# Kernel tuning notes

Measured on AMD Instinct MI355X. Metric: run time of the kernel, lower is better.

## Reference

```python
import jax, jax.numpy as jnp
import numpy as np

N_CLASS = 126
C = N_CLASS + 2      # START tag = C-2, STOP tag = C-1
B, T = 128, 512
NEG_BIG = -100000.0  # transition mask value from the torch init
NEG_INIT = -10000.0  # alpha init value


def setup_inputs() -> dict:
    key = jax.random.key(0)
    k1, k2, k3, k4 = jax.random.split(key, 4)
    feats = jax.random.normal(k1, (B, T, C), dtype=jnp.float32)
    # contiguous prefix masks (valid lengths in [1, T]) as the CRF scoring assumes
    lengths = jax.random.randint(k2, (B,), 1, T + 1)
    mask = (jnp.arange(T)[None, :] < lengths[:, None]).astype(jnp.int32)
    tags = jax.random.randint(k3, (B, T), 0, N_CLASS)  # real tags exclude START/STOP
    trans = jax.random.normal(k4, (C, C), dtype=jnp.float32)
    trans = trans.at[:, C - 2].set(NEG_BIG)  # nothing transitions INTO start
    trans = trans.at[C - 1, :].set(NEG_BIG)  # nothing transitions OUT of stop
    return {"feats": feats, "mask": mask, "tags": tags, "transitions": trans}


def _forward_alg_batch(feats, mask, trans):
    # log-partition via (logsumexp, +) semiring scan over time
    Bc, Tc, Cc = feats.shape
    alpha0 = jnp.full((Bc, Cc), NEG_INIT, feats.dtype).at[:, Cc - 2].set(0.0)
    maskb = mask.astype(bool)

    def step(alpha, xs):
        feat_t, m_t = xs                                   # [B,C], [B]
        smat = alpha[:, :, None] + feat_t[:, None, :] + trans[None]  # [B,C,C]: i->j
        new = jax.nn.logsumexp(smat, axis=1)               # [B,C]
        return jnp.where(m_t[:, None], new, alpha), None

    alpha, _ = jax.lax.scan(
        step, alpha0, (jnp.swapaxes(feats, 0, 1), jnp.swapaxes(maskb, 0, 1))
    )
    last = jax.nn.logsumexp(alpha + trans[:, Cc - 1][None, :], axis=1)  # to STOP
    return jnp.sum(last)


def _score_sentence_batch(feats, tags, mask, trans):
    Bc, Tc, Cc = feats.shape
    seq_len = mask.astype(jnp.int32).sum(1)                # [B]
    r = jnp.arange(Bc)
    start = jnp.full((Bc, 1), Cc - 2, tags.dtype)
    stop = jnp.full((Bc, 1), Cc - 1, tags.dtype)
    pad_start = jnp.concatenate([start, tags], axis=1)     # [B,T+1]
    pad_stop = jnp.concatenate([tags, stop], axis=1)       # [B,T+1]
    pad_stop = pad_stop.at[r, seq_len].set(Cc - 1)         # transition to STOP at end
    t = trans[pad_start, pad_stop]                          # [B,T+1]
    t_score = jnp.sum(jnp.cumsum(t, axis=1)[r, seq_len])
    f = jnp.take_along_axis(feats, tags[:, :, None], axis=2)[..., 0]  # [B,T]
    f_score = jnp.sum(jnp.where(mask.astype(bool), f, 0.0))
    return t_score + f_score


def reference(feats, mask, tags, transitions):
    # CRFTagger.calculate_loss with use_crf=True: NLL / batch_size
    nll = _forward_alg_batch(feats, mask, transitions) - _score_sentence_batch(
        feats, tags, mask, transitions
    )
    return nll / feats.shape[0]
```

## Files before the change

### kernel.cpp

```cpp
#include <hip/hip_runtime.h>


#define BB   128
#define TT   512
#define CC   128
#define NTHR 512
#define PF   4
#define WS_STRIDE 320

typedef float v2f __attribute__((ext_vector_type(2)));

__device__ __forceinline__ void bar_nodrain() {
    asm volatile("s_waitcnt lgkmcnt(0)\n\ts_barrier" ::: "memory");
}

template<int CTRL>
__device__ __forceinline__ float dpp_xadd(float x) {
    const int y = __builtin_amdgcn_update_dpp(0, __float_as_int(x), CTRL, 0xF, 0xF, true);
    return x + __int_as_float(y);
}

__device__ __forceinline__ float red8(float x) {
    x = dpp_xadd<0xB1>(x);
    x = dpp_xadd<0x4E>(x);
    x = dpp_xadd<0x141>(x);
    return x;
}

__global__ __launch_bounds__(NTHR) void crf_scan(
    const float* __restrict__ feats,
    const int*   __restrict__ mask,
    const int*   __restrict__ tags,
    const float* __restrict__ trans,
    float*       __restrict__ ws)
{
    const int bb  = blockIdx.x >> 1;
    const int dir = blockIdx.x & 1;
    const int tid = threadIdx.x;
    const int jp  = tid >> 3;
    const int sub = tid & 7;
    const int j0  = jp * 2;
    const int j1  = j0 + 1;
    const int wid = tid >> 6;

    __shared__ __align__(16) float buf[2][CC];
    __shared__ float wred[8];

    const int myM = mask[bb * TT + tid];
    const int len = __syncthreads_count(myM);

    if (dir == 0) {
        float sc = 0.0f;
        if (myM) {
            const int tg = tags[bb * TT + tid];
            sc += feats[((size_t)(bb * TT + tid)) * CC + tg];
            sc += (tid == 0) ? trans[(CC - 2) * CC + tg]
                             : trans[tags[bb * TT + tid - 1] * CC + tg];
            const int nm = (tid == TT - 1) ? 0 : mask[bb * TT + tid + 1];
            if (!nm) sc += trans[tg * CC + (CC - 1)];
        }
        #pragma unroll
        for (int o = 1; o <= 32; o <<= 1) sc += __shfl_xor(sc, o);
        if ((tid & 63) == 0) wred[wid] = sc;
        __syncthreads();
        if (tid == 0) {
            float s = 0.0f;
            #pragma unroll
            for (int k = 0; k < 8; ++k) s += wred[k];
            atomicAdd(&ws[1], s);
        }
    }

    const int M      = len >> 1;
    const int nB     = len - M;
    const int nSteps = dir ? nB : M;

    const float* fb = feats + (size_t)bb * TT * CC;

    const int s2 = sub >> 1;
    int kkA[4];
    v2f F0v[8], F1v[8];
    #pragma unroll
    for (int k = 0; k < 4; ++k) {
        const int kk = (k + s2) & 3;
        kkA[k] = kk;
        const int r = sub * 16 + kk * 4;
        if (dir == 0) {
            #pragma unroll
            for (int m = 0; m < 2; ++m) {
                const int r0 = r + 2 * m;
                const float2 ta = *(const float2*)&trans[(size_t)(r0    ) * CC + j0];
                const float2 tb = *(const float2*)&trans[(size_t)(r0 + 1) * CC + j0];
                v2f e0, e1;
                e0.x = __expf(ta.x); e0.y = __expf(tb.x);
                e1.x = __expf(ta.y); e1.y = __expf(tb.y);
                F0v[2 * k + m] = e0;
                F1v[2 * k + m] = e1;
            }
        } else {
            const float4 u0 = *(const float4*)&trans[(size_t)j0 * CC + r];
            const float4 u1 = *(const float4*)&trans[(size_t)j1 * CC + r];
            v2f e;
            e.x = __expf(u0.x); e.y = __expf(u0.y); F0v[2 * k]     = e;
            e.x = __expf(u0.z); e.y = __expf(u0.w); F0v[2 * k + 1] = e;
            e.x = __expf(u1.x); e.y = __expf(u1.y); F1v[2 * k]     = e;
            e.x = __expf(u1.z); e.y = __expf(u1.w); F1v[2 * k + 1] = e;
        }
    }

    if (tid < CC) {
        if (dir == 0) {
            buf[0][tid] = (tid == CC - 2) ? 1.0f : 0.0f;
        } else {
            buf[0][tid] = __expf(trans[(size_t)tid * CC + (CC - 1)])
                        * __expf(fb[(size_t)(len - 1) * CC + tid]);
        }
    }

    float2 fx[PF];
    #pragma unroll
    for (int k = 0; k < PF; ++k) {
        int tg;
        if (dir == 0) tg = k;
        else { tg = len - 2 - k; tg = (tg > 0) ? tg : 0; }
        fx[k] = *(const float2*)&fb[(size_t)tg * CC + j0];
    }

    const float* pb0 = &buf[0][sub * 16];
    const float* pb1 = &buf[1][sub * 16];

    float S = 0.0f;
    const int nUp = (nSteps + 3) & ~3;

    for (int tc = 0; tc < nUp; tc += 4) {
        #pragma unroll
        for (int k = 0; k < 4; ++k) {
            const int it  = tc + k;
            const int par = k & 1;
            bar_nodrain();
            const float4* q = (const float4*)(par ? pb1 : pb0);
            float c = 1.0f;
            if (k == 3) c = buf[1][0];

            v2f a0 = {0.f, 0.f}, a1 = {0.f, 0.f};
            v2f b0 = {0.f, 0.f}, b1 = {0.f, 0.f};
            #pragma unroll
            for (int kq = 0; kq < 4; ++kq) {
                const float4 P = q[kkA[kq]];
                v2f P01; P01.x = P.x; P01.y = P.y;
                v2f P23; P23.x = P.z; P23.y = P.w;
                a0 = __builtin_elementwise_fma(F0v[2 * kq],     P01, a0);
                a1 = __builtin_elementwise_fma(F0v[2 * kq + 1], P23, a1);
                b0 = __builtin_elementwise_fma(F1v[2 * kq],     P01, b0);
                b1 = __builtin_elementwise_fma(F1v[2 * kq + 1], P23, b1);
            }
            a0 += a1; b0 += b1;
            float s0 = red8(a0.x + a0.y);
            float s1 = red8(b0.x + b0.y);

            const bool noMul = (dir != 0) && (it == nSteps - 1);
            const float m0 = noMul ? 1.0f : __expf(fx[k].x);
            const float m1 = noMul ? 1.0f : __expf(fx[k].y);

            float v0, v1;
            if (k == 3) {
                const float rinv = __builtin_amdgcn_rcpf(c);
                v0 = m0 * s0 * rinv;
                v1 = m1 * s1 * rinv;
            } else {
                v0 = m0 * s0;
                v1 = m1 * s1;
            }

            int tn;
            if (dir == 0) { tn = it + PF;           tn = (tn < TT) ? tn : (TT - 1); }
            else          { tn = len - 2 - (it + PF); tn = (tn > 0) ? tn : 0; }
            fx[k] = *(const float2*)&fb[(size_t)tn * CC + j0];

            if (it < nSteps) {
                if (k == 3) S += __logf(c);
                if (sub == 0) {
                    float2 w2; w2.x = v0; w2.y = v1;
                    *(float2*)&buf[par ^ 1][j0] = w2;
                }
            }
        }
    }

    __syncthreads();
    float* resv = ws + 16 + (size_t)bb * WS_STRIDE + dir * 128;
    if (sub == 0) {
        const float2 uu = *(const float2*)&buf[nSteps & 1][j0];
        *(float2*)&resv[j0] = uu;
    }
    if (tid == 0) ws[16 + (size_t)bb * WS_STRIDE + 256 + dir] = S;
}

__global__ void crf_join(const float* __restrict__ ws, float* __restrict__ acc)
{
    const int b = blockIdx.x;
    const int i = threadIdx.x;
    const float* base = ws + 16 + (size_t)b * WS_STRIDE;
    float z = base[i] * base[128 + i] + base[64 + i] * base[192 + i];
    #pragma unroll
    for (int o = 1; o <= 32; o <<= 1) z += __shfl_xor(z, o);
    if (i == 0) atomicAdd(&acc[0], __logf(z) + base[256] + base[257]);
}

__global__ void crf_final(const float* __restrict__ acc, float* __restrict__ out)
{
    out[0] = (acc[0] - acc[1]) * (1.0f / (float)BB);
}

extern "C" void kernel_launch(void* const* d_in, const int* in_sizes, int n_in,
                              void* d_out, int out_size, void* d_ws, size_t ws_size,
                              hipStream_t stream)
{
    const float* feats = (const float*)d_in[0];
    const int*   mask  = (const int*)d_in[1];
    const int*   tags  = (const int*)d_in[2];
    const float* trans = (const float*)d_in[3];
    float* out = (float*)d_out;
    float* ws  = (float*)d_ws;

    hipMemsetAsync(ws, 0, 2 * sizeof(float), stream);
    crf_scan<<<BB * 2, NTHR, 0, stream>>>(feats, mask, tags, trans, ws);
    crf_join<<<BB, 64, 0, stream>>>(ws, ws);
    crf_final<<<1, 1, 0, stream>>>(ws, out);
}
```

Before: 166.8 us.

## Run each CRF scan direction in a single wavefront with register-resident transitions

Replaces the 512-thread block (8 waves, each lane holding a 16-row slice plus a DPP reduction and a block barrier every step) with one 64-lane wavefront per (batch, direction). Each lane keeps a full 128-row column pair of exp(transitions) in registers and reads the whole alpha vector from LDS, so per-step barriers and cross-lane reductions disappear. The memset and the two epilogue kernels are merged into one single-block epilogue that also subtracts a per-batch gold score stored in the workspace instead of using atomics. In exchange each lane does 8x more FMAs per step and holds 256 floats in registers, and only 256 wavefronts are launched, which risks spills and long serial step latency.

Measured after the change: 385.9 us. 131% more time.

```diff
diff --git a/kernel.cpp b/kernel.cpp
--- a/kernel.cpp
+++ b/kernel.cpp
@@ -4,130 +4,107 @@
 #define BB   128
 #define TT   512
 #define CC   128
-#define NTHR 512
 #define PF   4
 #define WS_STRIDE 320
 
 typedef float v2f __attribute__((ext_vector_type(2)));
 
-__device__ __forceinline__ void bar_nodrain() {
-    asm volatile("s_waitcnt lgkmcnt(0)\n\ts_barrier" ::: "memory");
-}
-
-template<int CTRL>
-__device__ __forceinline__ float dpp_xadd(float x) {
-    const int y = __builtin_amdgcn_update_dpp(0, __float_as_int(x), CTRL, 0xF, 0xF, true);
-    return x + __int_as_float(y);
-}
-
-__device__ __forceinline__ float red8(float x) {
-    x = dpp_xadd<0xB1>(x);
-    x = dpp_xadd<0x4E>(x);
-    x = dpp_xadd<0x141>(x);
-    return x;
-}
-
-__global__ __launch_bounds__(NTHR) void crf_scan(
+__device__ __forceinline__ void wait_lds() {
+    asm volatile("s_waitcnt lgkmcnt(0)" ::: "memory");
+}
+
+__global__ __launch_bounds__(64, 1) void crf_scan(
     const float* __restrict__ feats,
     const int*   __restrict__ mask,
     const int*   __restrict__ tags,
     const float* __restrict__ trans,
     float*       __restrict__ ws)
 {
-    const int bb  = blockIdx.x >> 1;
-    const int dir = blockIdx.x & 1;
-    const int tid = threadIdx.x;
-    const int jp  = tid >> 3;
-    const int sub = tid & 7;
-    const int j0  = jp * 2;
-    const int j1  = j0 + 1;
-    const int wid = tid >> 6;
+    const int bid  = blockIdx.x;
+    const int bb   = bid >> 1;
+    const int dir  = bid & 1;
+    const int lane = threadIdx.x;
+    const int j0   = lane * 2;
+    const int j1   = j0 + 1;
 
     __shared__ __align__(16) float buf[2][CC];
-    __shared__ float wred[8];
-
-    const int myM = mask[bb * TT + tid];
-    const int len = __syncthreads_count(myM);
-
+
+    const int base = bb * TT;
+
+    int len = 0;
+    int mvals[8];
+    #pragma unroll
+    for (int c2 = 0; c2 < 8; ++c2) {
+        mvals[c2] = mask[base + c2 * 64 + lane];
+        len += __popcll(__ballot(mvals[c2] != 0));
+    }
     if (dir == 0) {
         float sc = 0.0f;
-        if (myM) {
-            const int tg = tags[bb * TT + tid];
-            sc += feats[((size_t)(bb * TT + tid)) * CC + tg];
-            sc += (tid == 0) ? trans[(CC - 2) * CC + tg]
-                             : trans[tags[bb * TT + tid - 1] * CC + tg];
-            const int nm = (tid == TT - 1) ? 0 : mask[bb * TT + tid + 1];
-            if (!nm) sc += trans[tg * CC + (CC - 1)];
+        #pragma unroll
+        for (int c2 = 0; c2 < 8; ++c2) {
+            const int t = c2 * 64 + lane;
+            if (mvals[c2]) {
+                const int tg = tags[base + t];
+                sc += feats[((size_t)(base + t)) * CC + tg];
+                sc += (t == 0) ? trans[(CC - 2) * CC + tg]
+                               : trans[tags[base + t - 1] * CC + tg];
+                const int nm = (t == TT - 1) ? 0 : mask[base + t + 1];
+                if (!nm) sc += trans[tg * CC + (CC - 1)];
+            }
         }
         #pragma unroll
         for (int o = 1; o <= 32; o <<= 1) sc += __shfl_xor(sc, o);
-        if ((tid & 63) == 0) wred[wid] = sc;
-        __syncthreads();
-        if (tid == 0) {
-            float s = 0.0f;
-            #pragma unroll
-            for (int k = 0; k < 8; ++k) s += wred[k];
-            atomicAdd(&ws[1], s);
-        }
-    }
-
+        if (lane == 0) ws[16 + (size_t)bb * WS_STRIDE + 258] = sc;
+    }
+
+    v2f F0[64], F1[64];
+    if (dir == 0) {
+        #pragma unroll
+        for (int rr = 0; rr < 64; ++rr) {
+            const float2 ta = *(const float2*)&trans[(size_t)(2 * rr    ) * CC + j0];
+            const float2 tb = *(const float2*)&trans[(size_t)(2 * rr + 1) * CC + j0];
+            v2f e0; e0.x = __expf(ta.x); e0.y = __expf(tb.x); F0[rr] = e0;
+            v2f e1; e1.x = __expf(ta.y); e1.y = __expf(tb.y); F1[rr] = e1;
+        }
+    } else {
+        #pragma unroll
+        for (int q = 0; q < 32; ++q) {
+            const float4 u0 = *(const float4*)&trans[(size_t)j0 * CC + 4 * q];
+            const float4 u1 = *(const float4*)&trans[(size_t)j1 * CC + 4 * q];
+            v2f e;
+            e.x = __expf(u0.x); e.y = __expf(u0.y); F0[2 * q]     = e;
+            e.x = __expf(u0.z); e.y = __expf(u0.w); F0[2 * q + 1] = e;
+            e.x = __expf(u1.x); e.y = __expf(u1.y); F1[2 * q]     = e;
+            e.x = __expf(u1.z); e.y = __expf(u1.w); F1[2 * q + 1] = e;
+        }
+    }
+
+    const float* fb = feats + (size_t)base * CC;
     const int M      = len >> 1;
     const int nB     = len - M;
     const int nSteps = dir ? nB : M;
 
-    const float* fb = feats + (size_t)bb * TT * CC;
-
-    const int s2 = sub >> 1;
-    int kkA[4];
-    v2f F0v[8], F1v[8];
-    #pragma unroll
-    for (int k = 0; k < 4; ++k) {
-        const int kk = (k + s2) & 3;
-        kkA[k] = kk;
-        const int r = sub * 16 + kk * 4;
+    {
+        float2 w;
         if (dir == 0) {
-            #pragma unroll
-            for (int m = 0; m < 2; ++m) {
-                const int r0 = r + 2 * m;
-                const float2 ta = *(const float2*)&trans[(size_t)(r0    ) * CC + j0];
-                const float2 tb = *(const float2*)&trans[(size_t)(r0 + 1) * CC + j0];
-                v2f e0, e1;
-                e0.x = __expf(ta.x); e0.y = __expf(tb.x);
-                e1.x = __expf(ta.y); e1.y = __expf(tb.y);
-                F0v[2 * k + m] = e0;
-                F1v[2 * k + m] = e1;
-            }
+            w.x = (j0 == CC - 2) ? 1.0f : 0.0f;
+            w.y = (j1 == CC - 2) ? 1.0f : 0.0f;
         } else {
-            const float4 u0 = *(const float4*)&trans[(size_t)j0 * CC + r];
-            const float4 u1 = *(const float4*)&trans[(size_t)j1 * CC + r];
-            v2f e;
-            e.x = __expf(u0.x); e.y = __expf(u0.y); F0v[2 * k]     = e;
-            e.x = __expf(u0.z); e.y = __expf(u0.w); F0v[2 * k + 1] = e;
-            e.x = __expf(u1.x); e.y = __expf(u1.y); F1v[2 * k]     = e;
-            e.x = __expf(u1.z); e.y = __expf(u1.w); F1v[2 * k + 1] = e;
-        }
-    }
-
-    if (tid < CC) {
-        if (dir == 0) {
-            buf[0][tid] = (tid == CC - 2) ? 1.0f : 0.0f;
-        } else {
-            buf[0][tid] = __expf(trans[(size_t)tid * CC + (CC - 1)])
-                        * __expf(fb[(size_t)(len - 1) * CC + tid]);
-        }
-    }
+            const float2 ff = *(const float2*)&fb[(size_t)(len - 1) * CC + j0];
+            w.x = __expf(trans[(size_t)j0 * CC + (CC - 1)]) * __expf(ff.x);
+            w.y = __expf(trans[(size_t)j1 * CC + (CC - 1)]) * __expf(ff.y);
+        }
+        *(float2*)&buf[0][j0] = w;
+    }
+    wait_lds();
 
     float2 fx[PF];
     #pragma unroll
     for (int k = 0; k < PF; ++k) {
-        int tg;
-        if (dir == 0) tg = k;
-        else { tg = len - 2 - k; tg = (tg > 0) ? tg : 0; }
+        int tg = dir ? (len - 2 - k) : k;
+        tg = (tg > 0) ? tg : 0;
         fx[k] = *(const float2*)&fb[(size_t)tg * CC + j0];
     }
-
-    const float* pb0 = &buf[0][sub * 16];
-    const float* pb1 = &buf[1][sub * 16];
 
     float S = 0.0f;
     const int nUp = (nSteps + 3) & ~3;
@@ -137,79 +114,79 @@
         for (int k = 0; k < 4; ++k) {
             const int it  = tc + k;
             const int par = k & 1;
-            bar_nodrain();
-            const float4* q = (const float4*)(par ? pb1 : pb0);
-            float c = 1.0f;
-            if (k == 3) c = buf[1][0];
+            const float* q = &buf[par][0];
 
             v2f a0 = {0.f, 0.f}, a1 = {0.f, 0.f};
             v2f b0 = {0.f, 0.f}, b1 = {0.f, 0.f};
+            float u0val = 1.0f;
             #pragma unroll
-            for (int kq = 0; kq < 4; ++kq) {
-                const float4 P = q[kkA[kq]];
-                v2f P01; P01.x = P.x; P01.y = P.y;
-                v2f P23; P23.x = P.z; P23.y = P.w;
-                a0 = __builtin_elementwise_fma(F0v[2 * kq],     P01, a0);
-                a1 = __builtin_elementwise_fma(F0v[2 * kq + 1], P23, a1);
-                b0 = __builtin_elementwise_fma(F1v[2 * kq],     P01, b0);
-                b1 = __builtin_elementwise_fma(F1v[2 * kq + 1], P23, b1);
+            for (int qq = 0; qq < 32; ++qq) {
+                const float4 P = *(const float4*)(q + qq * 4);
+                if (qq == 0) u0val = P.x;
+                v2f U01; U01.x = P.x; U01.y = P.y;
+                v2f U23; U23.x = P.z; U23.y = P.w;
+                a0 = __builtin_elementwise_fma(F0[2 * qq],     U01, a0);
+                a1 = __builtin_elementwise_fma(F0[2 * qq + 1], U23, a1);
+                b0 = __builtin_elementwise_fma(F1[2 * qq],     U01, b0);
+                b1 = __builtin_elementwise_fma(F1[2 * qq + 1], U23, b1);
             }
             a0 += a1; b0 += b1;
-            float s0 = red8(a0.x + a0.y);
-            float s1 = red8(b0.x + b0.y);
+            const float s0 = a0.x + a0.y;
+            const float s1 = b0.x + b0.y;
 
             const bool noMul = (dir != 0) && (it == nSteps - 1);
-            const float m0 = noMul ? 1.0f : __expf(fx[k].x);
-            const float m1 = noMul ? 1.0f : __expf(fx[k].y);
+            const float e0f = noMul ? 1.0f : __expf(fx[k].x);
+            const float e1f = noMul ? 1.0f : __expf(fx[k].y);
 
             float v0, v1;
             if (k == 3) {
-                const float rinv = __builtin_amdgcn_rcpf(c);
-                v0 = m0 * s0 * rinv;
-                v1 = m1 * s1 * rinv;
+                const float rinv = __builtin_amdgcn_rcpf(u0val);
+                v0 = e0f * s0 * rinv;
+                v1 = e1f * s1 * rinv;
             } else {
-                v0 = m0 * s0;
-                v1 = m1 * s1;
-            }
-
-            int tn;
-            if (dir == 0) { tn = it + PF;           tn = (tn < TT) ? tn : (TT - 1); }
-            else          { tn = len - 2 - (it + PF); tn = (tn > 0) ? tn : 0; }
+                v0 = e0f * s0;
+                v1 = e1f * s1;
+            }
+
+            int tn = dir ? (len - 2 - (it + PF)) : (it + PF);
+            tn = dir ? ((tn > 0) ? tn : 0) : ((tn < TT) ? tn : (TT - 1));
             fx[k] = *(const float2*)&fb[(size_t)tn * CC + j0];
 
             if (it < nSteps) {
-                if (k == 3) S += __logf(c);
-                if (sub == 0) {
-                    float2 w2; w2.x = v0; w2.y = v1;
-                    *(float2*)&buf[par ^ 1][j0] = w2;
-                }
-            }
-        }
-    }
-
-    __syncthreads();
+                if (k == 3) S += __logf(u0val);
+                float2 w2; w2.x = v0; w2.y = v1;
+                *(float2*)&buf[par ^ 1][j0] = w2;
+            }
+            wait_lds();
+        }
+    }
+
+    const float2 uu = *(const float2*)&buf[nSteps & 1][j0];
     float* resv = ws + 16 + (size_t)bb * WS_STRIDE + dir * 128;
-    if (sub == 0) {
-        const float2 uu = *(const float2*)&buf[nSteps & 1][j0];
-        *(float2*)&resv[j0] = uu;
-    }
-    if (tid == 0) ws[16 + (size_t)bb * WS_STRIDE + 256 + dir] = S;
-}
-
-__global__ void crf_join(const float* __restrict__ ws, float* __restrict__ acc)
+    *(float2*)&resv[j0] = uu;
+    if (lane == 0) ws[16 + (size_t)bb * WS_STRIDE + 256 + dir] = S;
+}
+
+__global__ void crf_epi(const float* __restrict__ ws, float* __restrict__ out)
 {
-    const int b = blockIdx.x;
-    const int i = threadIdx.x;
-    const float* base = ws + 16 + (size_t)b * WS_STRIDE;
-    float z = base[i] * base[128 + i] + base[64 + i] * base[192 + i];
-    #pragma unroll
-    for (int o = 1; o <= 32; o <<= 1) z += __shfl_xor(z, o);
-    if (i == 0) atomicAdd(&acc[0], __logf(z) + base[256] + base[257]);
-}
-
-__global__ void crf_final(const float* __restrict__ acc, float* __restrict__ out)
-{
-    out[0] = (acc[0] - acc[1]) * (1.0f / (float)BB);
+    const int lane = threadIdx.x;
+    float r = 0.0f;
+    #pragma unroll
+    for (int h = 0; h < 2; ++h) {
+        const int b = lane * 2 + h;
+        const float* base = ws + 16 + (size_t)b * WS_STRIDE;
+        float dot = 0.0f;
+        #pragma unroll 8
+        for (int i = 0; i < 128; i += 4) {
+            const float4 av = *(const float4*)&base[i];
+            const float4 bv = *(const float4*)&base[128 + i];
+            dot += av.x * bv.x + av.y * bv.y + av.z * bv.z + av.w * bv.w;
+        }
+        r += __logf(dot) + base[256] + base[257] - base[258];
+    }
+    #pragma unroll
+    for (int o = 1; o <= 32; o <<= 1) r += __shfl_xor(r, o);
+    if (lane == 0) out[0] = r * (1.0f / (float)BB);
 }
 
 extern "C" void kernel_launch(void* const* d_in, const int* in_sizes, int n_in,
@@ -223,8 +200,6 @@
     float* out = (float*)d_out;
     float* ws  = (float*)d_ws;
 
-    hipMemsetAsync(ws, 0, 2 * sizeof(float), stream);
-    crf_scan<<<BB * 2, NTHR, 0, stream>>>(feats, mask, tags, trans, ws);
-    crf_join<<<BB, 64, 0, stream>>>(ws, ws);
-    crf_final<<<1, 1, 0, stream>>>(ws, out);
-}
+    crf_scan<<<BB * 2, 64, 0, stream>>>(feats, mask, tags, trans, ws);
+    crf_epi<<<1, 64, 0, stream>>>(ws, out);
+}
```

## Merge join and final kernels into one epilogue and drop memset and atomics

Applied to the files above, without the earlier changes.

Replaces the memset plus the join and final kernels with a single one-wave epilogue kernel. Each block's gold score is now written to a per-batch workspace slot instead of being atomically accumulated. The transition exponentials are held in named scalar registers kept live with empty asm barriers, and the end-of-scan __syncthreads becomes a lighter barrier. The aim is to cut launch count and atomic traffic, at the cost of a serial single-wave reduction over all batches.

Measured after the change: 169.2 us. Within noise of the previous version (+1.5%).

```diff
diff --git a/kernel.cpp b/kernel.cpp
--- a/kernel.cpp
+++ b/kernel.cpp
@@ -12,6 +12,11 @@
 
 __device__ __forceinline__ void bar_nodrain() {
     asm volatile("s_waitcnt lgkmcnt(0)\n\ts_barrier" ::: "memory");
+}
+
+__device__ __forceinline__ float kreg(float x) {
+    asm volatile("" : "+v"(x));
+    return x;
 }
 
 template<int CTRL>
@@ -67,67 +72,61 @@
             float s = 0.0f;
             #pragma unroll
             for (int k = 0; k < 8; ++k) s += wred[k];
-            atomicAdd(&ws[1], s);
-        }
-    }
-
+            ws[16 + (size_t)bb * WS_STRIDE + 258] = s;
+        }
+    }
+
+    const int sR = dir ? 1 : CC;
+    const int sJ = dir ? CC : 1;
+    const int s2 = sub >> 1;
+    const int c0 = (0 + s2) & 3, c1 = (1 + s2) & 3;
+    const int c2 = (2 + s2) & 3, c3 = (3 + s2) & 3;
+
+    v2f Ea0, Eb0, Ec0, Ed0, Ea1, Eb1, Ec1, Ed1;
+    v2f Ea2, Eb2, Ec2, Ed2, Ea3, Eb3, Ec3, Ed3;
+#define INITE(K, CK) { \
+    const int r = sub * 16 + (CK) * 4; \
+    Ea##K.x = __expf(trans[(size_t)(r    ) * sR + (size_t)j0 * sJ]); \
+    Ea##K.y = __expf(trans[(size_t)(r + 1) * sR + (size_t)j0 * sJ]); \
+    Eb##K.x = __expf(trans[(size_t)(r + 2) * sR + (size_t)j0 * sJ]); \
+    Eb##K.y = __expf(trans[(size_t)(r + 3) * sR + (size_t)j0 * sJ]); \
+    Ec##K.x = __expf(trans[(size_t)(r    ) * sR + (size_t)j1 * sJ]); \
+    Ec##K.y = __expf(trans[(size_t)(r + 1) * sR + (size_t)j1 * sJ]); \
+    Ed##K.x = __expf(trans[(size_t)(r + 2) * sR + (size_t)j1 * sJ]); \
+    Ed##K.y = __expf(trans[(size_t)(r + 3) * sR + (size_t)j1 * sJ]); }
+    INITE(0, c0) INITE(1, c1) INITE(2, c2) INITE(3, c3)
+#undef INITE
+#define OPQ(K) { \
+    Ea##K.x = kreg(Ea##K.x); Ea##K.y = kreg(Ea##K.y); \
+    Eb##K.x = kreg(Eb##K.x); Eb##K.y = kreg(Eb##K.y); \
+    Ec##K.x = kreg(Ec##K.x); Ec##K.y = kreg(Ec##K.y); \
+    Ed##K.x = kreg(Ed##K.x); Ed##K.y = kreg(Ed##K.y); }
+    OPQ(0) OPQ(1) OPQ(2) OPQ(3)
+#undef OPQ
+
+    const float* fb = feats + (size_t)(bb * TT) * CC;
     const int M      = len >> 1;
     const int nB     = len - M;
     const int nSteps = dir ? nB : M;
 
-    const float* fb = feats + (size_t)bb * TT * CC;
-
-    const int s2 = sub >> 1;
-    int kkA[4];
-    v2f F0v[8], F1v[8];
-    #pragma unroll
-    for (int k = 0; k < 4; ++k) {
-        const int kk = (k + s2) & 3;
-        kkA[k] = kk;
-        const int r = sub * 16 + kk * 4;
-        if (dir == 0) {
-            #pragma unroll
-            for (int m = 0; m < 2; ++m) {
-                const int r0 = r + 2 * m;
-                const float2 ta = *(const float2*)&trans[(size_t)(r0    ) * CC + j0];
-                const float2 tb = *(const float2*)&trans[(size_t)(r0 + 1) * CC + j0];
-                v2f e0, e1;
-                e0.x = __expf(ta.x); e0.y = __expf(tb.x);
-                e1.x = __expf(ta.y); e1.y = __expf(tb.y);
-                F0v[2 * k + m] = e0;
-                F1v[2 * k + m] = e1;
-            }
-        } else {
-            const float4 u0 = *(const float4*)&trans[(size_t)j0 * CC + r];
-            const float4 u1 = *(const float4*)&trans[(size_t)j1 * CC + r];
-            v2f e;
-            e.x = __expf(u0.x); e.y = __expf(u0.y); F0v[2 * k]     = e;
-            e.x = __expf(u0.z); e.y = __expf(u0.w); F0v[2 * k + 1] = e;
-            e.x = __expf(u1.x); e.y = __expf(u1.y); F1v[2 * k]     = e;
-            e.x = __expf(u1.z); e.y = __expf(u1.w); F1v[2 * k + 1] = e;
-        }
-    }
-
     if (tid < CC) {
-        if (dir == 0) {
-            buf[0][tid] = (tid == CC - 2) ? 1.0f : 0.0f;
-        } else {
-            buf[0][tid] = __expf(trans[(size_t)tid * CC + (CC - 1)])
+        float v;
+        if (dir == 0) v = (tid == CC - 2) ? 1.0f : 0.0f;
+        else          v = __expf(trans[(size_t)tid * CC + (CC - 1)])
                         * __expf(fb[(size_t)(len - 1) * CC + tid]);
-        }
+        buf[0][tid] = v;
     }
 
     float2 fx[PF];
     #pragma unroll
     for (int k = 0; k < PF; ++k) {
-        int tg;
-        if (dir == 0) tg = k;
-        else { tg = len - 2 - k; tg = (tg > 0) ? tg : 0; }
+        int tg = dir ? (len - 2 - k) : k;
+        tg = (tg > 0) ? tg : 0;
         fx[k] = *(const float2*)&fb[(size_t)tg * CC + j0];
     }
 
-    const float* pb0 = &buf[0][sub * 16];
-    const float* pb1 = &buf[1][sub * 16];
+    const float4* pb0c = (const float4*)&buf[0][sub * 16];
+    const float4* pb1c = (const float4*)&buf[1][sub * 16];
 
     float S = 0.0f;
     const int nUp = (nSteps + 3) & ~3;
@@ -138,43 +137,47 @@
             const int it  = tc + k;
             const int par = k & 1;
             bar_nodrain();
-            const float4* q = (const float4*)(par ? pb1 : pb0);
+            const float4* qb = par ? pb1c : pb0c;
             float c = 1.0f;
             if (k == 3) c = buf[1][0];
 
+            const float4 P0 = qb[c0];
+            const float4 P1 = qb[c1];
+            const float4 P2 = qb[c2];
+            const float4 P3 = qb[c3];
+
             v2f a0 = {0.f, 0.f}, a1 = {0.f, 0.f};
             v2f b0 = {0.f, 0.f}, b1 = {0.f, 0.f};
-            #pragma unroll
-            for (int kq = 0; kq < 4; ++kq) {
-                const float4 P = q[kkA[kq]];
-                v2f P01; P01.x = P.x; P01.y = P.y;
-                v2f P23; P23.x = P.z; P23.y = P.w;
-                a0 = __builtin_elementwise_fma(F0v[2 * kq],     P01, a0);
-                a1 = __builtin_elementwise_fma(F0v[2 * kq + 1], P23, a1);
-                b0 = __builtin_elementwise_fma(F1v[2 * kq],     P01, b0);
-                b1 = __builtin_elementwise_fma(F1v[2 * kq + 1], P23, b1);
-            }
+#define DOT(K, P) { \
+            v2f U01; U01.x = (P).x; U01.y = (P).y; \
+            v2f U23; U23.x = (P).z; U23.y = (P).w; \
+            a0 = __builtin_elementwise_fma(Ea##K, U01, a0); \
+            a1 = __builtin_elementwise_fma(Eb##K, U23, a1); \
+            b0 = __builtin_elementwise_fma(Ec##K, U01, b0); \
+            b1 = __builtin_elementwise_fma(Ed##K, U23, b1); }
+            DOT(0, P0) DOT(1, P1) DOT(2, P2) DOT(3, P3)
+#undef DOT
             a0 += a1; b0 += b1;
             float s0 = red8(a0.x + a0.y);
             float s1 = red8(b0.x + b0.y);
 
             const bool noMul = (dir != 0) && (it == nSteps - 1);
-            const float m0 = noMul ? 1.0f : __expf(fx[k].x);
-            const float m1 = noMul ? 1.0f : __expf(fx[k].y);
+            const float e0f = noMul ? 1.0f : __expf(fx[k].x);
+            const float e1f = noMul ? 1.0f : __expf(fx[k].y);
 
             float v0, v1;
             if (k == 3) {
                 const float rinv = __builtin_amdgcn_rcpf(c);
-                v0 = m0 * s0 * rinv;
-                v1 = m1 * s1 * rinv;
+                v0 = e0f * s0 * rinv;
+                v1 = e1f * s1 * rinv;
             } else {
-                v0 = m0 * s0;
-                v1 = m1 * s1;
+                v0 = e0f * s0;
+                v1 = e1f * s1;
             }
 
-            int tn;
-            if (dir == 0) { tn = it + PF;           tn = (tn < TT) ? tn : (TT - 1); }
-            else          { tn = len - 2 - (it + PF); tn = (tn > 0) ? tn : 0; }
+            int tn = dir ? (len - 2 - (it + PF)) : (it + PF);
+            tn = (tn > 0) ? tn : 0;
+            tn = (tn < TT - 1) ? tn : (TT - 1);
             fx[k] = *(const float2*)&fb[(size_t)tn * CC + j0];
 
             if (it < nSteps) {
@@ -187,7 +190,7 @@
         }
     }
 
-    __syncthreads();
+    bar_nodrain();
     float* resv = ws + 16 + (size_t)bb * WS_STRIDE + dir * 128;
     if (sub == 0) {
         const float2 uu = *(const float2*)&buf[nSteps & 1][j0];
@@ -196,20 +199,26 @@
     if (tid == 0) ws[16 + (size_t)bb * WS_STRIDE + 256 + dir] = S;
 }
 
-__global__ void crf_join(const float* __restrict__ ws, float* __restrict__ acc)
+__global__ void crf_epi(const float* __restrict__ ws, float* __restrict__ out)
 {
-    const int b = blockIdx.x;
-    const int i = threadIdx.x;
-    const float* base = ws + 16 + (size_t)b * WS_STRIDE;
-    float z = base[i] * base[128 + i] + base[64 + i] * base[192 + i];
+    const int lane = threadIdx.x;
+    float r = 0.0f;
     #pragma unroll
-    for (int o = 1; o <= 32; o <<= 1) z += __shfl_xor(z, o);
-    if (i == 0) atomicAdd(&acc[0], __logf(z) + base[256] + base[257]);
-}
-
-__global__ void crf_final(const float* __restrict__ acc, float* __restrict__ out)
-{
-    out[0] = (acc[0] - acc[1]) * (1.0f / (float)BB);
+    for (int h = 0; h < 2; ++h) {
+        const int b = lane * 2 + h;
+        const float* base = ws + 16 + (size_t)b * WS_STRIDE;
+        float dot = 0.0f;
+        #pragma unroll 8
+        for (int i = 0; i < 128; i += 4) {
+            const float4 av = *(const float4*)&base[i];
+            const float4 bv = *(const float4*)&base[128 + i];
+            dot += av.x * bv.x + av.y * bv.y + av.z * bv.z + av.w * bv.w;
+        }
+        r += __logf(dot) + base[256] + base[257] - base[258];
+    }
+    #pragma unroll
+    for (int o = 1; o <= 32; o <<= 1) r += __shfl_xor(r, o);
+    if (lane == 0) out[0] = r * (1.0f / (float)BB);
 }
 
 extern "C" void kernel_launch(void* const* d_in, const int* in_sizes, int n_in,
@@ -223,8 +232,6 @@
     float* out = (float*)d_out;
     float* ws  = (float*)d_ws;
 
-    hipMemsetAsync(ws, 0, 2 * sizeof(float), stream);
     crf_scan<<<BB * 2, NTHR, 0, stream>>>(feats, mask, tags, trans, ws);
-    crf_join<<<BB, 64, 0, stream>>>(ws, ws);
-    crf_final<<<1, 1, 0, stream>>>(ws, out);
-}
+    crf_epi<<<1, 64, 0, stream>>>(ws, out);
+}
```
